# Performance work log

Hardware: AMD Instinct MI355X
Metric: run time of the kernel (lower is better)

## Reference

```python
import jax, jax.numpy as jnp
import numpy as np

# Standard SMPL kinematic tree (24 joints); parents[0] = -1 (root)
PARENTS = np.array([-1, 0, 0, 0, 1, 2, 3, 4, 5, 6, 7, 8, 9, 9, 9, 12, 13, 14, 16, 17, 18, 19, 20, 21], dtype=np.int32)
B, V, J, NSHAPE, NPOSEBASIS = 512, 6890, 24, 10, 207


def setup_inputs() -> dict:
    key = jax.random.key(0)
    ks = jax.random.split(key, 9)
    poses = jax.random.normal(ks[0], (B, J * 3), dtype=jnp.float32) * 0.2
    shapes = jax.random.normal(ks[1], (B, NSHAPE), dtype=jnp.float32)
    Rh = jax.random.normal(ks[2], (B, 3), dtype=jnp.float32) * 0.2
    Th = jax.random.normal(ks[3], (B, 3), dtype=jnp.float32)
    v_template = jax.random.normal(ks[4], (V, 3), dtype=jnp.float32)
    shapedirs = jax.random.normal(ks[5], (V, 3, NSHAPE), dtype=jnp.float32) * 0.01
    posedirs = jax.random.normal(ks[6], (NPOSEBASIS, V * 3), dtype=jnp.float32) * 0.01
    jr = jax.random.uniform(ks[7], (J, V), dtype=jnp.float32)
    J_regressor = jr / jnp.sum(jr, axis=1, keepdims=True)
    w = jax.random.uniform(ks[8], (V, J), dtype=jnp.float32)
    weights = w / jnp.sum(w, axis=1, keepdims=True)
    return {"poses": poses, "shapes": shapes, "Rh": Rh, "Th": Th,
            "v_template": v_template, "shapedirs": shapedirs, "posedirs": posedirs,
            "J_regressor": J_regressor, "weights": weights}


def batch_rodrigues(rot_vecs):
    # rot_vecs: (N,3) -> (N,3,3); matches smplx batch_rodrigues
    angle = jnp.linalg.norm(rot_vecs + 1e-8, axis=1, keepdims=True)  # (N,1)
    rd = rot_vecs / angle
    cos = jnp.cos(angle)[:, :, None]
    sin = jnp.sin(angle)[:, :, None]
    rx, ry, rz = rd[:, 0], rd[:, 1], rd[:, 2]
    zeros = jnp.zeros_like(rx)
    K = jnp.stack([zeros, -rz, ry, rz, zeros, -rx, -ry, rx, zeros], axis=1).reshape(-1, 3, 3)
    ident = jnp.eye(3, dtype=rot_vecs.dtype)[None]
    return ident + sin * K + (1.0 - cos) * jnp.matmul(K, K)


def smpl_forward(poses, shapes, Rh, Th, v_template, shapedirs, posedirs, J_regressor, weights):
    bn = poses.shape[0]
    # shape blendshapes: v_shaped (B,V,3)
    v_shaped = v_template[None] + jnp.einsum('bl,vdl->bvd', shapes, shapedirs)
    # rest-pose joints (B,J,3)
    Jrest = jnp.einsum('jv,bvd->bjd', J_regressor, v_shaped)
    # per-joint rotation matrices
    rot_mats = batch_rodrigues(poses.reshape(-1, 3)).reshape(bn, J, 3, 3)
    # pose blendshapes
    ident = jnp.eye(3, dtype=poses.dtype)
    pose_feature = (rot_mats[:, 1:] - ident).reshape(bn, -1)  # (B,207)
    v_posed = v_shaped + jnp.matmul(pose_feature, posedirs).reshape(bn, V, 3)
    # kinematic chain rigid transforms
    rel_joints = jnp.concatenate([Jrest[:, :1], Jrest[:, 1:] - Jrest[:, PARENTS[1:]]], axis=1)
    bottom = jnp.tile(jnp.array([0., 0., 0., 1.], dtype=poses.dtype), (bn, J, 1, 1))
    tmats = jnp.concatenate([jnp.concatenate([rot_mats, rel_joints[..., None]], axis=-1), bottom], axis=-2)  # (B,J,4,4)
    chain = [tmats[:, 0]]
    for i in range(1, J):
        chain.append(jnp.matmul(chain[PARENTS[i]], tmats[:, i]))
    transforms = jnp.stack(chain, axis=1)  # (B,J,4,4)
    # remove rest-pose joint location from transforms
    tj = jnp.einsum('bjik,bjk->bji', transforms[:, :, :3, :3], Jrest)
    A = transforms.at[:, :, :3, 3].add(-tj)
    # linear blend skinning
    T = jnp.einsum('vj,bjik->bvik', weights, A)  # (B,V,4,4)
    verts = jnp.einsum('bvik,bvk->bvi', T[:, :, :3, :3], v_posed) + T[:, :, :3, 3]
    # global rotation + translation
    rot = batch_rodrigues(Rh)  # (B,3,3)
    vertices = jnp.einsum('bij,bvj->bvi', rot, verts) + Th[:, None]
    return vertices


def reference(poses, shapes, Rh, Th, v_template, shapedirs, posedirs, J_regressor, weights):
    return smpl_forward(poses, shapes, Rh, Th, v_template, shapedirs, posedirs, J_regressor, weights)
```

## Files before the change

kernel.cpp:

```cpp
#include <hip/hip_runtime.h>


#define BN 512
#define NV 6890
#define NVP 6912
#define NJ 24
#define NS 10
#define NP 207
#define PSTR 208
#define KP 224
#define NPAD 20736
#define BB 8
#define TV 256

#define WS_JSP 0
#define WS_G   6400
#define WS_PF  153856
#define WS_A1  12800
#define WS_A2  127488
#define WS_WT  324096
#define WS_BT  545280
#define FULL_NEED ((size_t)10380288)

typedef unsigned short u16;
typedef short bf16x8 __attribute__((ext_vector_type(8)));
typedef float f32x4  __attribute__((ext_vector_type(4)));

__constant__ int c_par[NJ] = {-1,0,0,0,1,2,3,4,5,6,7,8,9,9,9,12,13,14,16,17,18,19,20,21};

__device__ __forceinline__ u16 f2bf(float f){
    union { float f; unsigned i; } x; x.f = f;
    unsigned r = x.i + 0x7fffu + ((x.i >> 16) & 1u);
    return (u16)(r >> 16);
}

__global__ __launch_bounds__(256) void k_prep(const float* __restrict__ jreg,
                                              const float* __restrict__ vt,
                                              const float* __restrict__ sd,
                                              const float* __restrict__ pd,
                                              const float* __restrict__ wts,
                                              float* __restrict__ ws,
                                              u16* __restrict__ bt,
                                              u16* __restrict__ wt,
                                              int full){
    __shared__ __align__(16) float s_red[4][33];
    __shared__ __align__(16) u16 s_tile[32][65];
    int bid = blockIdx.x;
    int t = threadIdx.x;

    if(bid < 192){
        int j = bid >> 3, s = bid & 7;
        int v0 = s*864, v1 = min(NV, v0+864);
        float acc[33];
        #pragma unroll
        for(int k=0;k<33;k++) acc[k]=0.f;
        for(int v=v0+t; v<v1; v+=256){
            float jr = jreg[j*NV+v];
            #pragma unroll
            for(int d=0;d<3;d++) acc[d] = fmaf(jr, vt[v*3+d], acc[d]);
            const float2* sp = (const float2*)(sd + (size_t)v*30);
            #pragma unroll
            for(int k=0;k<15;k++){
                float2 s2 = sp[k];
                acc[3+2*k]   = fmaf(jr, s2.x, acc[3+2*k]);
                acc[3+2*k+1] = fmaf(jr, s2.y, acc[3+2*k+1]);
            }
        }
        int lane = t & 63, wv = t >> 6;
        #pragma unroll
        for(int k=0;k<33;k++){
            float val = acc[k];
            #pragma unroll
            for(int off=32; off; off>>=1) val += __shfl_down(val, off, 64);
            if(lane==0) s_red[wv][k]=val;
        }
        __syncthreads();
        if(t<33) ws[WS_JSP + (j*8+s)*33 + t] = s_red[0][t]+s_red[1][t]+s_red[2][t]+s_red[3][t];
    } else if(bid < 2460){
        if(!full) return;
        int bid2 = bid - 192;
        int n0 = (bid2 % 324) * 64;
        int k0 = (bid2 / 324) * 32;
        int nl = t & 63, kb = (t>>6)*8;
        int n = n0 + nl;
        #pragma unroll
        for(int i=0;i<8;i++){
            int k = k0 + kb + i;
            float v = 0.f;
            if(n < NV*3){
                if(k < NP)           v = pd[(size_t)k*(NV*3) + n];
                else if(k < NP+NS)   v = sd[(size_t)(n/3)*30 + (n%3)*10 + (k-NP)];
            }
            s_tile[kb+i][nl] = f2bf(v);
        }
        __syncthreads();
        int nl2 = t >> 2, kc = t & 3;
        union { u16 s[8]; uint4 q; } u;
        #pragma unroll
        for(int i=0;i<8;i++) u.s[i] = s_tile[kc*8+i][nl2];
        int ng = n0 + nl2;
        int v = ng/3, d = ng%3;
        int chunk = (k0>>3) + kc;
        *(uint4*)(bt + (((size_t)d*28 + chunk)*NVP + v)*8) = u.q;
    } else {
        if(!full) return;
        int v = (bid - 2460)*256 + t;
        if(v >= NVP) return;
        union { u16 s[32]; uint4 q[4]; } u;
        #pragma unroll
        for(int j=0;j<24;j++) u.s[j] = (v<NV) ? f2bf(wts[(size_t)v*24+j]) : (u16)0;
        #pragma unroll
        for(int j=24;j<32;j++) u.s[j]=0;
        #pragma unroll
        for(int c=0;c<4;c++)
            *(uint4*)(wt + ((size_t)c*NVP + v)*8) = u.q[c];
    }
}

__global__ __launch_bounds__(64) void k_chain(const float* __restrict__ poses,
                                              const float* __restrict__ shapes,
                                              const float* __restrict__ Rh,
                                              float* __restrict__ ws,
                                              u16* __restrict__ a1,
                                              u16* __restrict__ a2,
                                              int full){
    int b = blockIdx.x;
    int t = threadIdx.x;
    __shared__ float R[25][9];
    __shared__ float sh[NS];
    __shared__ float js[792];
    __shared__ float jrest[NJ][3];
    __shared__ float rel[NJ][3];
    __shared__ float chR[NJ][9];
    __shared__ float chT[NJ][3];
    __shared__ float Gs[NJ][12];

    if(t<25){
        float x,y,z;
        if(t<24){ x=poses[b*72+t*3]; y=poses[b*72+t*3+1]; z=poses[b*72+t*3+2]; }
        else    { x=Rh[b*3];         y=Rh[b*3+1];         z=Rh[b*3+2]; }
        float ax=x+1e-8f, ay=y+1e-8f, az=z+1e-8f;
        float ang = sqrtf(ax*ax+ay*ay+az*az);
        float inv = 1.f/ang;
        float rx=x*inv, ry=y*inv, rz=z*inv;
        float s = sinf(ang), c = cosf(ang), oc = 1.f - c;
        R[t][0]=1.f+oc*(-rz*rz-ry*ry); R[t][1]=-s*rz+oc*(rx*ry);      R[t][2]= s*ry+oc*(rx*rz);
        R[t][3]= s*rz+oc*(rx*ry);      R[t][4]=1.f+oc*(-rz*rz-rx*rx); R[t][5]=-s*rx+oc*(ry*rz);
        R[t][6]=-s*ry+oc*(rx*rz);      R[t][7]= s*rx+oc*(ry*rz);      R[t][8]=1.f+oc*(-ry*ry-rx*rx);
    }
    if(t<NS) sh[t]=shapes[b*NS+t];
    for(int idx=t; idx<792; idx+=64){
        int j = idx/33, e = idx%33;
        float a = 0.f;
        #pragma unroll
        for(int s=0;s<8;s++) a += ws[WS_JSP + (j*8+s)*33 + e];
        js[idx]=a;
    }
    __syncthreads();

    for(int idx=t; idx<KP; idx+=64){
        float v = 0.f;
        if(idx<NP){
            int j = 1 + idx/9, e = idx%9;
            v = R[j][e] - ((e==0||e==4||e==8)?1.f:0.f);
        } else if(idx<NP+NS) v = sh[idx-NP];
        if(full){ a1[(((size_t)(idx>>3))*BN + b)*8 + (idx&7)] = f2bf(v); }
        else if(idx<PSTR) ws[WS_PF + b*PSTR + idx] = (idx<NP)?v:0.f;
    }
    if(t<NJ){
        #pragma unroll
        for(int d=0;d<3;d++){
            float a = js[t*33 + d];
            #pragma unroll
            for(int l=0;l<NS;l++) a = fmaf(sh[l], js[t*33 + 3 + d*10 + l], a);
            jrest[t][d]=a;
        }
    }
    __syncthreads();
    if(t<NJ){
        int p = c_par[t];
        #pragma unroll
        for(int d=0;d<3;d++) rel[t][d] = (t==0) ? jrest[0][d] : jrest[t][d]-jrest[p][d];
    }
    __syncthreads();
    if(t<9) chR[0][t]=R[0][t];
    if(t<3) chT[0][t]=rel[0][t];
    __syncthreads();
    for(int i=1;i<NJ;i++){
        if(t<12){
            int r=t>>2, cc=t&3, p=c_par[i];
            if(cc<3){
                chR[i][r*3+cc] = chR[p][r*3+0]*R[i][0*3+cc] + chR[p][r*3+1]*R[i][1*3+cc] + chR[p][r*3+2]*R[i][2*3+cc];
            } else {
                chT[i][r] = chR[p][r*3+0]*rel[i][0] + chR[p][r*3+1]*rel[i][1] + chR[p][r*3+2]*rel[i][2] + chT[p][r];
            }
        }
        __syncthreads();
    }
    if(t<NJ){
        float rg[9];
        #pragma unroll
        for(int k=0;k<9;k++) rg[k]=R[24][k];
        float at[3];
        #pragma unroll
        for(int r=0;r<3;r++){
            float tj = chR[t][r*3+0]*jrest[t][0] + chR[t][r*3+1]*jrest[t][1] + chR[t][r*3+2]*jrest[t][2];
            at[r] = chT[t][r] - tj;
        }
        #pragma unroll
        for(int r=0;r<3;r++){
            #pragma unroll
            for(int cc=0;cc<3;cc++)
                Gs[t][r*4+cc] = rg[r*3+0]*chR[t][0*3+cc] + rg[r*3+1]*chR[t][1*3+cc] + rg[r*3+2]*chR[t][2*3+cc];
            Gs[t][r*4+3] = rg[r*3+0]*at[0] + rg[r*3+1]*at[1] + rg[r*3+2]*at[2];
        }
    }
    __syncthreads();
    if(full){
        for(int idx=t; idx<12*32; idx+=64){
            int e = idx>>5, k = idx&31;
            float v = (k<NJ) ? Gs[k][e] : 0.f;
            a2[((((size_t)e*4)+(k>>3))*BN + b)*8 + (k&7)] = f2bf(v);
        }
    } else if(t<NJ){
        float* g = &ws[WS_G + b*288 + t*12];
        #pragma unroll
        for(int e=0;e<12;e++) g[e] = Gs[t][e];
    }
}

__global__ __launch_bounds__(256) void k_fused(const u16* __restrict__ A1,
                                               const u16* __restrict__ A2,
                                               const u16* __restrict__ WT,
                                               const u16* __restrict__ BT,
                                               const float* __restrict__ vt,
                                               const float* __restrict__ th,
                                               float* __restrict__ out){
    int t = threadIdx.x;
    int w = t>>6, lane = t&63;
    int quad = lane>>4, l16 = lane&15;
    int v = blockIdx.y*64 + w*16 + l16;

    bf16x8 Bf[3][7];
    #pragma unroll
    for(int d=0;d<3;d++)
        #pragma unroll
        for(int s=0;s<7;s++)
            Bf[d][s] = *(const bf16x8*)(BT + (((size_t)d*28 + s*4 + quad)*NVP + v)*8);
    bf16x8 wf = *(const bf16x8*)(WT + ((size_t)quad*NVP + v)*8);
    float vt0=0.f, vt1=0.f, vt2=0.f;
    if(v<NV){ vt0=vt[v*3]; vt1=vt[v*3+1]; vt2=vt[v*3+2]; }
    f32x4 zz = {0.f,0.f,0.f,0.f};

    #pragma unroll 1
    for(int mi=0;mi<8;mi++){
        int m0 = blockIdx.x*128 + mi*16;
        int mrow = m0 + l16;
        f32x4 accP0=zz, accP1=zz, accP2=zz;
        #pragma unroll
        for(int s=0;s<7;s++){
            bf16x8 af = *(const bf16x8*)(A1 + (((size_t)s*4 + quad)*BN + mrow)*8);
            accP0 = __builtin_amdgcn_mfma_f32_16x16x32_bf16(af, Bf[0][s], accP0, 0,0,0);
            accP1 = __builtin_amdgcn_mfma_f32_16x16x32_bf16(af, Bf[1][s], accP1, 0,0,0);
            accP2 = __builtin_amdgcn_mfma_f32_16x16x32_bf16(af, Bf[2][s], accP2, 0,0,0);
        }
        f32x4 accT[12];
        #pragma unroll
        for(int e=0;e<12;e++){
            bf16x8 gf = *(const bf16x8*)(A2 + (((size_t)e*4 + quad)*BN + mrow)*8);
            accT[e] = __builtin_amdgcn_mfma_f32_16x16x32_bf16(gf, wf, zz, 0,0,0);
        }
        if(v < NV){
            #pragma unroll
            for(int r=0;r<4;r++){
                int b = m0 + quad*4 + r;
                float t0 = th[b*3+0], t1 = th[b*3+1], t2 = th[b*3+2];
                float p0 = accP0[r] + vt0;
                float p1 = accP1[r] + vt1;
                float p2 = accP2[r] + vt2;
                float o0 = fmaf(accT[0][r],p0, fmaf(accT[1][r],p1, fmaf(accT[2][r], p2, accT[3][r]))) + t0;
                float o1 = fmaf(accT[4][r],p0, fmaf(accT[5][r],p1, fmaf(accT[6][r], p2, accT[7][r]))) + t1;
                float o2 = fmaf(accT[8][r],p0, fmaf(accT[9][r],p1, fmaf(accT[10][r],p2, accT[11][r]))) + t2;
                float* op = out + ((size_t)b*NV + v)*3;
                op[0]=o0; op[1]=o1; op[2]=o2;
            }
        }
    }
}

__global__ __launch_bounds__(256) void k_main(const float* __restrict__ vt,
                                              const float* __restrict__ sd,
                                              const float* __restrict__ pd,
                                              const float* __restrict__ wts,
                                              const float* __restrict__ th,
                                              const float* __restrict__ shapes,
                                              const float* __restrict__ ws,
                                              float* __restrict__ out){
    __shared__ __align__(16) float pf_s[BB*PSTR];
    __shared__ __align__(16) float g_s[BB*288];
    __shared__ float th_s[BB*3];
    __shared__ float sh_s[BB*NS];
    int tid = threadIdx.x;
    int b0  = blockIdx.y * BB;
    int v   = blockIdx.x * TV + tid;

    for(int i=tid; i<BB*PSTR; i+=TV) pf_s[i] = ws[WS_PF + b0*PSTR + i];
    for(int i=tid; i<BB*288;  i+=TV) g_s[i]  = ws[WS_G  + b0*288  + i];
    if(tid<BB*3)  th_s[tid] = th[b0*3+tid];
    if(tid<BB*NS) sh_s[tid] = shapes[b0*NS+tid];
    __syncthreads();
    if(v>=NV) return;

    float sdv[30];
    {
        const float2* sp = (const float2*)(sd + (size_t)v*30);
        #pragma unroll
        for(int i=0;i<15;i++){ float2 s2 = sp[i]; sdv[2*i]=s2.x; sdv[2*i+1]=s2.y; }
    }
    float vt0=vt[v*3], vt1=vt[v*3+1], vt2=vt[v*3+2];
    float vp[BB][3];
    #pragma unroll
    for(int b=0;b<BB;b++){
        #pragma unroll
        for(int d=0;d<3;d++){
            float a = (d==0)?vt0:((d==1)?vt1:vt2);
            #pragma unroll
            for(int l=0;l<NS;l++) a = fmaf(sh_s[b*NS+l], sdv[d*10+l], a);
            vp[b][d]=a;
        }
    }
    const float* pcol = pd + (size_t)v*3;
    int p=0;
    for(; p<=NP-4; p+=4){
        float pdv[4][3];
        #pragma unroll
        for(int q=0;q<4;q++){
            size_t base = (size_t)(p+q)*(NV*3);
            pdv[q][0]=pcol[base]; pdv[q][1]=pcol[base+1]; pdv[q][2]=pcol[base+2];
        }
        #pragma unroll
        for(int b=0;b<BB;b++){
            float4 f = *(const float4*)&pf_s[b*PSTR+p];
            #pragma unroll
            for(int d=0;d<3;d++)
                vp[b][d] = fmaf(f.x,pdv[0][d], fmaf(f.y,pdv[1][d], fmaf(f.z,pdv[2][d], fmaf(f.w,pdv[3][d], vp[b][d]))));
        }
    }
    for(; p<NP; p++){
        size_t base=(size_t)p*(NV*3);
        float p0=pcol[base], p1=pcol[base+1], p2=pcol[base+2];
        #pragma unroll
        for(int b=0;b<BB;b++){
            float f = pf_s[b*PSTR+p];
            vp[b][0]=fmaf(f,p0,vp[b][0]); vp[b][1]=fmaf(f,p1,vp[b][1]); vp[b][2]=fmaf(f,p2,vp[b][2]);
        }
    }
    float w[24];
    {
        const float4* wp = (const float4*)(wts + (size_t)v*24);
        #pragma unroll
        for(int i=0;i<6;i++){
            float4 u = wp[i];
            w[i*4+0]=u.x; w[i*4+1]=u.y; w[i*4+2]=u.z; w[i*4+3]=u.w;
        }
    }
    #pragma unroll 1
    for(int b=0;b<BB;b++){
        float4 T0=make_float4(0.f,0.f,0.f,0.f), T1=T0, T2=T0;
        #pragma unroll
        for(int j=0;j<NJ;j++){
            float wj = w[j];
            const float4* g = (const float4*)&g_s[b*288 + j*12];
            float4 g0=g[0], g1=g[1], g2=g[2];
            T0.x=fmaf(wj,g0.x,T0.x); T0.y=fmaf(wj,g0.y,T0.y); T0.z=fmaf(wj,g0.z,T0.z); T0.w=fmaf(wj,g0.w,T0.w);
            T1.x=fmaf(wj,g1.x,T1.x); T1.y=fmaf(wj,g1.y,T1.y); T1.z=fmaf(wj,g1.z,T1.z); T1.w=fmaf(wj,g1.w,T1.w);
            T2.x=fmaf(wj,g2.x,T2.x); T2.y=fmaf(wj,g2.y,T2.y); T2.z=fmaf(wj,g2.z,T2.z); T2.w=fmaf(wj,g2.w,T2.w);
        }
        float x=vp[b][0], y=vp[b][1], z=vp[b][2];
        float ox = fmaf(T0.x,x, fmaf(T0.y,y, fmaf(T0.z,z, T0.w))) + th_s[b*3+0];
        float oy = fmaf(T1.x,x, fmaf(T1.y,y, fmaf(T1.z,z, T1.w))) + th_s[b*3+1];
        float oz = fmaf(T2.x,x, fmaf(T2.y,y, fmaf(T2.z,z, T2.w))) + th_s[b*3+2];
        size_t o = ((size_t)(b0+b)*NV + v)*3;
        out[o]=ox; out[o+1]=oy; out[o+2]=oz;
    }
}

extern "C" void kernel_launch(void* const* d_in, const int* in_sizes, int n_in,
                              void* d_out, int out_size, void* d_ws, size_t ws_size,
                              hipStream_t stream){
    const float* poses  = (const float*)d_in[0];
    const float* shapes = (const float*)d_in[1];
    const float* Rh     = (const float*)d_in[2];
    const float* Th     = (const float*)d_in[3];
    const float* vt     = (const float*)d_in[4];
    const float* sd     = (const float*)d_in[5];
    const float* pdirs  = (const float*)d_in[6];
    const float* jreg   = (const float*)d_in[7];
    const float* wts    = (const float*)d_in[8];
    float* ws  = (float*)d_ws;
    float* out = (float*)d_out;
    u16* u = (u16*)d_ws;
    int full = (ws_size >= FULL_NEED) ? 1 : 0;

    hipLaunchKernelGGL(k_prep, dim3(2487), dim3(256), 0, stream,
                       jreg, vt, sd, pdirs, wts, ws, u + WS_BT, u + WS_WT, full);
    hipLaunchKernelGGL(k_chain, dim3(BN), dim3(64), 0, stream, poses, shapes, Rh, ws,
                       u + WS_A1, u + WS_A2, full);
    if(full){
        hipLaunchKernelGGL(k_fused, dim3(BN/128, NVP/64), dim3(256), 0, stream,
                           u + WS_A1, u + WS_A2, u + WS_WT, u + WS_BT, vt, Th, out);
    } else {
        hipLaunchKernelGGL(k_main, dim3((NV+TV-1)/TV, BN/BB), dim3(256), 0, stream,
                           vt, sd, pdirs, wts, Th, shapes, ws, out);
    }
}
```

Before: 139.0 us.

## Fuse kinematic chain computation into MFMA skinning kernel via shared memory

The per-batch Rodrigues, joint regression, kinematic chain and bone-transform computation now runs inside the MFMA skinning kernel. Each block handles 32 batches and 256 vertices, and builds its bf16 A operands directly in LDS. This drops the separate k_chain launch and the global write/read of the A1/A2 operand buffers. In exchange the chain work is repeated in every vertex-block column, with 23 serial barrier steps at the start of each block. The kernel also uses about 117 KB of LDS, which likely limits it to one block per CU and leaves no other block to hide that preamble.

```diff
diff --git a/kernel.cpp b/kernel.cpp
--- a/kernel.cpp
+++ b/kernel.cpp
@@ -9,15 +9,12 @@
 #define NP 207
 #define PSTR 208
 #define KP 224
-#define NPAD 20736
 #define BB 8
 #define TV 256
 
 #define WS_JSP 0
 #define WS_G   6400
 #define WS_PF  153856
-#define WS_A1  12800
-#define WS_A2  127488
 #define WS_WT  324096
 #define WS_BT  545280
 #define FULL_NEED ((size_t)10380288)
@@ -117,13 +114,176 @@
     }
 }
 
+__global__ __launch_bounds__(256) void k_fused2(const float* __restrict__ poses,
+                                                const float* __restrict__ shapes,
+                                                const float* __restrict__ Rh,
+                                                const float* __restrict__ th,
+                                                const float* __restrict__ vt,
+                                                const float* __restrict__ ws,
+                                                const u16* __restrict__ WT,
+                                                const u16* __restrict__ BT,
+                                                float* __restrict__ out){
+    __shared__ float js[792];
+    __shared__ float Rl[32*226];
+    __shared__ float jre[32*73];
+    __shared__ float ch[32*289];
+    __shared__ __align__(16) u16 A1L[28*32*8];
+    __shared__ __align__(16) u16 A2L[12*4*32*8];
+
+    int t = threadIdx.x;
+    int m0 = blockIdx.x * 32;
+
+    for(int idx=t; idx<792; idx+=256){
+        int j = idx/33, e = idx%33;
+        float a = 0.f;
+        #pragma unroll
+        for(int s=0;s<8;s++) a += ws[WS_JSP + (j*8+s)*33 + e];
+        js[idx]=a;
+    }
+    for(int it=t; it<32*25; it+=256){
+        int b = it & 31, j = it >> 5;
+        int gb = m0 + b;
+        float x,y,z;
+        if(j<24){ x=poses[gb*72+j*3]; y=poses[gb*72+j*3+1]; z=poses[gb*72+j*3+2]; }
+        else    { x=Rh[gb*3];         y=Rh[gb*3+1];         z=Rh[gb*3+2]; }
+        float ax=x+1e-8f, ay=y+1e-8f, az=z+1e-8f;
+        float ang = sqrtf(ax*ax+ay*ay+az*az);
+        float inv = 1.f/ang;
+        float rx=x*inv, ry=y*inv, rz=z*inv;
+        float s = sinf(ang), c = cosf(ang), oc = 1.f - c;
+        float* R = &Rl[b*226 + j*9];
+        R[0]=1.f+oc*(-rz*rz-ry*ry); R[1]=-s*rz+oc*(rx*ry);      R[2]= s*ry+oc*(rx*rz);
+        R[3]= s*rz+oc*(rx*ry);      R[4]=1.f+oc*(-rz*rz-rx*rx); R[5]=-s*rx+oc*(ry*rz);
+        R[6]=-s*ry+oc*(rx*rz);      R[7]= s*rx+oc*(ry*rz);      R[8]=1.f+oc*(-ry*ry-rx*rx);
+    }
+    __syncthreads();
+    for(int it=t; it<32*224; it+=256){
+        int b = it & 31, idx = it >> 5;
+        float v = 0.f;
+        if(idx<NP){
+            int j = 1 + idx/9, e = idx%9;
+            v = Rl[b*226 + j*9 + e] - ((e==0||e==4||e==8)?1.f:0.f);
+        } else if(idx<NP+NS) v = shapes[(m0+b)*NS + idx-NP];
+        A1L[(idx>>3)*256 + b*8 + (idx&7)] = f2bf(v);
+    }
+    for(int it=t; it<32*72; it+=256){
+        int b = it & 31, rest = it >> 5;
+        int j = rest/3, d = rest%3;
+        float a = js[j*33 + d];
+        #pragma unroll
+        for(int l=0;l<NS;l++) a = fmaf(shapes[(m0+b)*NS+l], js[j*33 + 3 + d*10 + l], a);
+        jre[b*73 + j*3 + d] = a;
+    }
+    __syncthreads();
+    for(int it=t; it<32*12; it+=256){
+        int b = it & 31, e = it >> 5;
+        int r = e>>2, c = e&3;
+        ch[b*289 + e] = (c<3) ? Rl[b*226 + r*3 + c] : jre[b*73 + r];
+    }
+    __syncthreads();
+    for(int i=1;i<NJ;i++){
+        int p = c_par[i];
+        for(int it=t; it<32*12; it+=256){
+            int b = it & 31, e = it >> 5;
+            int r = e>>2, c = e&3;
+            const float* cp = &ch[b*289 + p*12 + r*4];
+            float acc;
+            if(c<3){
+                const float* Ri = &Rl[b*226 + i*9];
+                acc = cp[0]*Ri[c] + cp[1]*Ri[3+c] + cp[2]*Ri[6+c];
+            } else {
+                const float* ji = &jre[b*73 + i*3];
+                const float* jp = &jre[b*73 + p*3];
+                acc = cp[0]*(ji[0]-jp[0]) + cp[1]*(ji[1]-jp[1]) + cp[2]*(ji[2]-jp[2]) + cp[3];
+            }
+            ch[b*289 + i*12 + e] = acc;
+        }
+        __syncthreads();
+    }
+    for(int it=t; it<32*32; it+=256){
+        int b = it & 31, j = it >> 5;
+        if(j < NJ){
+            const float* rg = &Rl[b*226 + 24*9];
+            const float* cj = &ch[b*289 + j*12];
+            const float* jj = &jre[b*73 + j*3];
+            float at[3];
+            #pragma unroll
+            for(int r=0;r<3;r++)
+                at[r] = cj[r*4+3] - (cj[r*4+0]*jj[0] + cj[r*4+1]*jj[1] + cj[r*4+2]*jj[2]);
+            #pragma unroll
+            for(int r=0;r<3;r++){
+                #pragma unroll
+                for(int c=0;c<3;c++){
+                    float g = rg[r*3+0]*cj[0*4+c] + rg[r*3+1]*cj[1*4+c] + rg[r*3+2]*cj[2*4+c];
+                    A2L[(r*4+c)*1024 + (j>>3)*256 + b*8 + (j&7)] = f2bf(g);
+                }
+                float g3 = rg[r*3+0]*at[0] + rg[r*3+1]*at[1] + rg[r*3+2]*at[2];
+                A2L[(r*4+3)*1024 + (j>>3)*256 + b*8 + (j&7)] = f2bf(g3);
+            }
+        } else {
+            #pragma unroll
+            for(int e=0;e<12;e++)
+                A2L[e*1024 + 3*256 + b*8 + (j&7)] = 0;
+        }
+    }
+    __syncthreads();
+
+    int w = t>>6, lane = t&63, quad = lane>>4, l16 = lane&15;
+    f32x4 zz = {0.f,0.f,0.f,0.f};
+    #pragma unroll 1
+    for(int vi=0; vi<4; vi++){
+        int v = blockIdx.y*256 + vi*64 + w*16 + l16;
+        bf16x8 Bf[3][7];
+        #pragma unroll
+        for(int d=0;d<3;d++)
+            #pragma unroll
+            for(int s=0;s<7;s++)
+                Bf[d][s] = *(const bf16x8*)(BT + (((size_t)d*28 + s*4 + quad)*NVP + v)*8);
+        bf16x8 wf = *(const bf16x8*)(WT + ((size_t)quad*NVP + v)*8);
+        float vt0=0.f, vt1=0.f, vt2=0.f;
+        bool vok = (v < NV);
+        if(vok){ vt0=vt[v*3]; vt1=vt[v*3+1]; vt2=vt[v*3+2]; }
+
+        #pragma unroll
+        for(int mi=0;mi<2;mi++){
+            int mloc = mi*16 + l16;
+            f32x4 accP0=zz, accP1=zz, accP2=zz;
+            #pragma unroll
+            for(int s=0;s<7;s++){
+                bf16x8 af = *(const bf16x8*)&A1L[(s*4+quad)*256 + mloc*8];
+                accP0 = __builtin_amdgcn_mfma_f32_16x16x32_bf16(af, Bf[0][s], accP0, 0,0,0);
+                accP1 = __builtin_amdgcn_mfma_f32_16x16x32_bf16(af, Bf[1][s], accP1, 0,0,0);
+                accP2 = __builtin_amdgcn_mfma_f32_16x16x32_bf16(af, Bf[2][s], accP2, 0,0,0);
+            }
+            f32x4 accT[12];
+            #pragma unroll
+            for(int e=0;e<12;e++){
+                bf16x8 gf = *(const bf16x8*)&A2L[e*1024 + quad*256 + mloc*8];
+                accT[e] = __builtin_amdgcn_mfma_f32_16x16x32_bf16(gf, wf, zz, 0,0,0);
+            }
+            if(vok){
+                #pragma unroll
+                for(int r=0;r<4;r++){
+                    int b = m0 + mi*16 + quad*4 + r;
+                    float t0 = th[b*3+0], t1 = th[b*3+1], t2 = th[b*3+2];
+                    float p0 = accP0[r] + vt0;
+                    float p1 = accP1[r] + vt1;
+                    float p2 = accP2[r] + vt2;
+                    float o0 = fmaf(accT[0][r],p0, fmaf(accT[1][r],p1, fmaf(accT[2][r], p2, accT[3][r]))) + t0;
+                    float o1 = fmaf(accT[4][r],p0, fmaf(accT[5][r],p1, fmaf(accT[6][r], p2, accT[7][r]))) + t1;
+                    float o2 = fmaf(accT[8][r],p0, fmaf(accT[9][r],p1, fmaf(accT[10][r],p2, accT[11][r]))) + t2;
+                    float* op = out + ((size_t)b*NV + v)*3;
+                    op[0]=o0; op[1]=o1; op[2]=o2;
+                }
+            }
+        }
+    }
+}
+
 __global__ __launch_bounds__(64) void k_chain(const float* __restrict__ poses,
                                               const float* __restrict__ shapes,
                                               const float* __restrict__ Rh,
-                                              float* __restrict__ ws,
-                                              u16* __restrict__ a1,
-                                              u16* __restrict__ a2,
-                                              int full){
+                                              float* __restrict__ ws){
     int b = blockIdx.x;
     int t = threadIdx.x;
     __shared__ float R[25][9];
@@ -133,7 +293,6 @@
     __shared__ float rel[NJ][3];
     __shared__ float chR[NJ][9];
     __shared__ float chT[NJ][3];
-    __shared__ float Gs[NJ][12];
 
     if(t<25){
         float x,y,z;
@@ -157,15 +316,13 @@
         js[idx]=a;
     }
     __syncthreads();
-
-    for(int idx=t; idx<KP; idx+=64){
+    for(int idx=t; idx<PSTR; idx+=64){
         float v = 0.f;
         if(idx<NP){
             int j = 1 + idx/9, e = idx%9;
             v = R[j][e] - ((e==0||e==4||e==8)?1.f:0.f);
-        } else if(idx<NP+NS) v = sh[idx-NP];
-        if(full){ a1[(((size_t)(idx>>3))*BN + b)*8 + (idx&7)] = f2bf(v); }
-        else if(idx<PSTR) ws[WS_PF + b*PSTR + idx] = (idx<NP)?v:0.f;
+        }
+        ws[WS_PF + b*PSTR + idx] = v;
     }
     if(t<NJ){
         #pragma unroll
@@ -207,83 +364,13 @@
             float tj = chR[t][r*3+0]*jrest[t][0] + chR[t][r*3+1]*jrest[t][1] + chR[t][r*3+2]*jrest[t][2];
             at[r] = chT[t][r] - tj;
         }
+        float* g = &ws[WS_G + b*288 + t*12];
         #pragma unroll
         for(int r=0;r<3;r++){
             #pragma unroll
             for(int cc=0;cc<3;cc++)
-                Gs[t][r*4+cc] = rg[r*3+0]*chR[t][0*3+cc] + rg[r*3+1]*chR[t][1*3+cc] + rg[r*3+2]*chR[t][2*3+cc];
-            Gs[t][r*4+3] = rg[r*3+0]*at[0] + rg[r*3+1]*at[1] + rg[r*3+2]*at[2];
-        }
-    }
-    __syncthreads();
-    if(full){
-        for(int idx=t; idx<12*32; idx+=64){
-            int e = idx>>5, k = idx&31;
-            float v = (k<NJ) ? Gs[k][e] : 0.f;
-            a2[((((size_t)e*4)+(k>>3))*BN + b)*8 + (k&7)] = f2bf(v);
-        }
-    } else if(t<NJ){
-        float* g = &ws[WS_G + b*288 + t*12];
-        #pragma unroll
-        for(int e=0;e<12;e++) g[e] = Gs[t][e];
-    }
-}
-
-__global__ __launch_bounds__(256) void k_fused(const u16* __restrict__ A1,
-                                               const u16* __restrict__ A2,
-                                               const u16* __restrict__ WT,
-                                               const u16* __restrict__ BT,
-                                               const float* __restrict__ vt,
-                                               const float* __restrict__ th,
-                                               float* __restrict__ out){
-    int t = threadIdx.x;
-    int w = t>>6, lane = t&63;
-    int quad = lane>>4, l16 = lane&15;
-    int v = blockIdx.y*64 + w*16 + l16;
-
-    bf16x8 Bf[3][7];
-    #pragma unroll
-    for(int d=0;d<3;d++)
-        #pragma unroll
-        for(int s=0;s<7;s++)
-            Bf[d][s] = *(const bf16x8*)(BT + (((size_t)d*28 + s*4 + quad)*NVP + v)*8);
-    bf16x8 wf = *(const bf16x8*)(WT + ((size_t)quad*NVP + v)*8);
-    float vt0=0.f, vt1=0.f, vt2=0.f;
-    if(v<NV){ vt0=vt[v*3]; vt1=vt[v*3+1]; vt2=vt[v*3+2]; }
-    f32x4 zz = {0.f,0.f,0.f,0.f};
-
-    #pragma unroll 1
-    for(int mi=0;mi<8;mi++){
-        int m0 = blockIdx.x*128 + mi*16;
-        int mrow = m0 + l16;
-        f32x4 accP0=zz, accP1=zz, accP2=zz;
-        #pragma unroll
-        for(int s=0;s<7;s++){
-            bf16x8 af = *(const bf16x8*)(A1 + (((size_t)s*4 + quad)*BN + mrow)*8);
-            accP0 = __builtin_amdgcn_mfma_f32_16x16x32_bf16(af, Bf[0][s], accP0, 0,0,0);
-            accP1 = __builtin_amdgcn_mfma_f32_16x16x32_bf16(af, Bf[1][s], accP1, 0,0,0);
-            accP2 = __builtin_amdgcn_mfma_f32_16x16x32_bf16(af, Bf[2][s], accP2, 0,0,0);
-        }
-        f32x4 accT[12];
-        #pragma unroll
-        for(int e=0;e<12;e++){
-            bf16x8 gf = *(const bf16x8*)(A2 + (((size_t)e*4 + quad)*BN + mrow)*8);
-            accT[e] = __builtin_amdgcn_mfma_f32_16x16x32_bf16(gf, wf, zz, 0,0,0);
-        }
-        if(v < NV){
-            #pragma unroll
-            for(int r=0;r<4;r++){
-                int b = m0 + quad*4 + r;
-                float t0 = th[b*3+0], t1 = th[b*3+1], t2 = th[b*3+2];
-                float p0 = accP0[r] + vt0;
-                float p1 = accP1[r] + vt1;
-                float p2 = accP2[r] + vt2;
-                float o0 = fmaf(accT[0][r],p0, fmaf(accT[1][r],p1, fmaf(accT[2][r], p2, accT[3][r]))) + t0;
-                float o1 = fmaf(accT[4][r],p0, fmaf(accT[5][r],p1, fmaf(accT[6][r], p2, accT[7][r]))) + t1;
-                float o2 = fmaf(accT[8][r],p0, fmaf(accT[9][r],p1, fmaf(accT[10][r],p2, accT[11][r]))) + t2;
-                float* op = out + ((size_t)b*NV + v)*3;
-                op[0]=o0; op[1]=o1; op[2]=o2;
-            }
+                g[r*4+cc] = rg[r*3+0]*chR[t][0*3+cc] + rg[r*3+1]*chR[t][1*3+cc] + rg[r*3+2]*chR[t][2*3+cc];
+            g[r*4+3] = rg[r*3+0]*at[0] + rg[r*3+1]*at[1] + rg[r*3+2]*at[2];
         }
     }
 }
@@ -404,12 +491,11 @@
 
     hipLaunchKernelGGL(k_prep, dim3(2487), dim3(256), 0, stream,
                        jreg, vt, sd, pdirs, wts, ws, u + WS_BT, u + WS_WT, full);
-    hipLaunchKernelGGL(k_chain, dim3(BN), dim3(64), 0, stream, poses, shapes, Rh, ws,
-                       u + WS_A1, u + WS_A2, full);
     if(full){
-        hipLaunchKernelGGL(k_fused, dim3(BN/128, NVP/64), dim3(256), 0, stream,
-                           u + WS_A1, u + WS_A2, u + WS_WT, u + WS_BT, vt, Th, out);
+        hipLaunchKernelGGL(k_fused2, dim3(BN/32, NVP/256), dim3(256), 0, stream,
+                           poses, shapes, Rh, Th, vt, ws, u + WS_WT, u + WS_BT, out);
     } else {
+        hipLaunchKernelGGL(k_chain, dim3(BN), dim3(64), 0, stream, poses, shapes, Rh, ws);
         hipLaunchKernelGGL(k_main, dim3((NV+TV-1)/TV, BN/BB), dim3(256), 0, stream,
                            vt, sd, pdirs, wts, Th, shapes, ws, out);
     }
```

Result: slower. 165.6 us (+19.1%).
